# Kernel tuning notes

Hardware: AMD Instinct MI355X
Metric: run time of the kernel (lower is better)

Reference implementation:

```python
import jax, jax.numpy as jnp
import numpy as np

D, H = 1536, 16
HD = D // H            # head_dim = 96
ROPE_CH = HD // 2      # rope_channels_ratio=0.5 -> RoPE on last 48 channels
FF = 4 * D             # SwiGLU hidden
EPS = 1e-6
MAX_WAVELENGTH = 10000.0


def _ln(x):
    # LayerNorm, elementwise_affine=False, eps=1e-6
    m = jnp.mean(x, axis=-1, keepdims=True)
    v = jnp.var(x, axis=-1, keepdims=True)
    return (x - m) * jax.lax.rsqrt(v + EPS)


def _rms(x, w):
    # LlamaRMSNorm: fp32 internally
    xf = x.astype(jnp.float32)
    v = jnp.mean(jnp.square(xf), axis=-1, keepdims=True)
    return (w * (xf * jax.lax.rsqrt(v + EPS))).astype(x.dtype)


def _apply_rope(q, pos):
    # q: [B,H,S,hd], pos: [B,S]
    hd = q.shape[-1]
    frac = 2.0 * jnp.arange(hd // 2, dtype=jnp.float32) / hd
    timescale = MAX_WAVELENGTH ** frac                       # [hd/2]
    sin_inp = pos.astype(jnp.float32)[:, None, :, None] / timescale  # [B,1,S,hd/2]
    sin, cos = jnp.sin(sin_inp), jnp.cos(sin_inp)
    a, b = jnp.split(q, 2, axis=-1)
    out = jnp.concatenate([a * cos - b * sin, b * cos + a * sin], axis=-1)
    return out.astype(q.dtype)


def _rotary(x, pos, ch):
    # apply RoPE to the last `ch` channels of head_dim
    left, right = x[..., :-ch], x[..., -ch:]
    return jnp.concatenate([left, _apply_rope(right, pos)], axis=-1)


def _mod(x, shift, scale):
    # t2i_modulate: x * (1 + scale) + shift, cond broadcast over seq
    return x * (1.0 + scale[:, None, :]) + shift[:, None, :]


def setup_inputs() -> dict:
    key = jax.random.key(0)
    ks = jax.random.split(key, 32)
    B, Nx, Ny = 1, 2048, 256
    w = lambda k, shp: (0.02 * jax.random.normal(k, shp, dtype=jnp.float32))
    inp = {
        'x': jax.random.normal(ks[0], (B, Nx, D), dtype=jnp.float32),
        'y': jax.random.normal(ks[1], (B, Ny, D), dtype=jnp.float32),
        't': jax.random.normal(ks[2], (B, D), dtype=jnp.float32),
        'positions': jnp.arange(Nx, dtype=jnp.int32).reshape(B, Nx),
        'w_mod_x': w(ks[3], (D, 6 * D)), 'b_mod_x': jnp.zeros((6 * D,), jnp.float32),
        'w_mod_y': w(ks[4], (D, 6 * D)), 'b_mod_y': jnp.zeros((6 * D,), jnp.float32),
        'w_qkv_x': w(ks[5], (D, 3 * D)), 'b_qkv_x': jnp.zeros((3 * D,), jnp.float32),
        'w_qkv_y': w(ks[6], (D, 3 * D)), 'b_qkv_y': jnp.zeros((3 * D,), jnp.float32),
        'qn_x': jnp.ones((HD,), jnp.float32), 'kn_x': jnp.ones((HD,), jnp.float32),
        'qn_y': jnp.ones((HD,), jnp.float32), 'kn_y': jnp.ones((HD,), jnp.float32),
        'w_proj_x': w(ks[7], (D, D)), 'b_proj_x': jnp.zeros((D,), jnp.float32),
        'w_proj_y': w(ks[8], (D, D)), 'b_proj_y': jnp.zeros((D,), jnp.float32),
        'w1_x': w(ks[9], (D, FF)), 'w2_x': w(ks[10], (D, FF)), 'w3_x': w(ks[11], (FF, D)),
        'w1_y': w(ks[12], (D, FF)), 'w2_y': w(ks[13], (D, FF)), 'w3_y': w(ks[14], (FF, D)),
    }
    return inp


def reference(x, y, t, positions,
              w_mod_x, b_mod_x, w_mod_y, b_mod_y,
              w_qkv_x, b_qkv_x, w_qkv_y, b_qkv_y,
              qn_x, kn_x, qn_y, kn_y,
              w_proj_x, b_proj_x, w_proj_y, b_proj_y,
              w1_x, w2_x, w3_x, w1_y, w2_y, w3_y):
    B, Nx, _ = x.shape
    Ny = y.shape[1]
    st = jax.nn.silu(t)
    sh1x, sc1x, g1x, sh2x, sc2x, g2x = jnp.split(st @ w_mod_x + b_mod_x, 6, axis=-1)
    sh1y, sc1y, g1y, sh2y, sc2y, g2y = jnp.split(st @ w_mod_y + b_mod_y, 6, axis=-1)

    def qkv(z, w, b, qn, kn, pos):
        q, k, v = jnp.split(z @ w + b, 3, axis=-1)
        r = lambda u: u.reshape(B, -1, H, HD).transpose(0, 2, 1, 3)  # [B,H,S,hd]
        q, k, v = r(q), r(k), r(v)
        q, k = _rms(q, qn), _rms(k, kn)
        if pos is not None:
            q, k = _rotary(q, pos, ROPE_CH), _rotary(k, pos, ROPE_CH)
        return q, k, v

    qx, kx, vx = qkv(_mod(_ln(x), sh1x, sc1x), w_qkv_x, b_qkv_x, qn_x, kn_x, positions)
    qy, ky, vy = qkv(_mod(_ln(y), sh1y, sc1y), w_qkv_y, b_qkv_y, qn_y, kn_y, None)

    q = jnp.concatenate([qx, qy], axis=2)
    k = jnp.concatenate([kx, ky], axis=2)
    v = jnp.concatenate([vx, vy], axis=2)
    scores = jnp.einsum('bhqd,bhkd->bhqk', q, k) * (HD ** -0.5)
    attn = jax.nn.softmax(scores, axis=-1)
    o = jnp.einsum('bhqk,bhkd->bhqd', attn, v)
    o = o.transpose(0, 2, 1, 3).reshape(B, Nx + Ny, D)
    ox, oy = o[:, :Nx], o[:, Nx:]

    x = x + g1x[:, None, :] * (ox @ w_proj_x + b_proj_x)
    y = y + g1y[:, None, :] * (oy @ w_proj_y + b_proj_y)

    def ffn(z, w1, w2, w3):
        return (jax.nn.silu(z @ w1) * (z @ w2)) @ w3

    x = x + g2x[:, None, :] * ffn(_mod(_ln(x), sh2x, sc2x), w1_x, w2_x, w3_x)
    y = y + g2y[:, None, :] * ffn(_mod(_ln(y), sh2y, sc2y), w1_y, w2_y, w3_y)
    return jnp.concatenate([x, y], axis=1)
```

## Files before the change

### kernel.cpp

```cpp
#include <hip/hip_runtime.h>
#include <hip/hip_bf16.h>

#define D_  1536
#define H_  16
#define HD_ 96
#define NX_ 2048
#define NY_ 256
#define NT_ 2304
#define FF_ 6144
#define EPS_ 1e-6f

typedef unsigned short u16;
typedef unsigned int   u32;
typedef short short8 __attribute__((ext_vector_type(8)));
typedef float f32x4  __attribute__((ext_vector_type(4)));
typedef unsigned short u16x4 __attribute__((ext_vector_type(4)));

__device__ __forceinline__ u16 f2bf(float f){
    u32 u = __float_as_uint(f);
    return (u16)((u + 0x7fffu + ((u >> 16) & 1u)) >> 16);
}
__device__ __forceinline__ float bf2f(u16 h){ return __uint_as_float(((u32)h) << 16); }

__device__ __forceinline__ void gll16(const void* g, void* l){
    __builtin_amdgcn_global_load_lds(
        (const __attribute__((address_space(1))) unsigned int*)g,
        (__attribute__((address_space(3))) unsigned int*)l, 16, 0, 0);
}

__global__ __launch_bounds__(256) void transpose_k(
    const float* __restrict__ Wx, const float* __restrict__ Wy,
    u16* __restrict__ Ox, u16* __restrict__ Oy, int K, int N)
{
    const float* W = blockIdx.y ? Wy : Wx;
    u16* O = blockIdx.y ? Oy : Ox;
    int tn_cnt = N >> 5;
    int tk = blockIdx.x / tn_cnt, tn = blockIdx.x % tn_cnt;
    __shared__ float tile[32][33];
    int t = threadIdx.x;
    {
        int k = t >> 3, n4 = (t & 7) * 4;
        float4 v = *(const float4*)&W[(size_t)(tk*32 + k) * N + tn*32 + n4];
        tile[k][n4+0] = v.x; tile[k][n4+1] = v.y;
        tile[k][n4+2] = v.z; tile[k][n4+3] = v.w;
    }
    __syncthreads();
    {
        int n = t >> 3, k4 = (t & 7) * 4;
        u16x4 r;
        #pragma unroll
        for (int i = 0; i < 4; i++) r[i] = f2bf(tile[k4+i][n]);
        *(u16x4*)&O[(size_t)(tn*32 + n) * K + tk*32 + k4] = r;
    }
}

__global__ __launch_bounds__(256) void modvec_k(
    const float* __restrict__ t_in,
    const float* __restrict__ w_mod_x, const float* __restrict__ b_mod_x,
    const float* __restrict__ w_mod_y, const float* __restrict__ b_mod_y,
    float* __restrict__ modx, float* __restrict__ mody)
{
    __shared__ float st[D_];
    int tid = threadIdx.x;
    for (int k = tid; k < D_; k += 256){
        float v = t_in[k];
        st[k] = v / (1.f + __expf(-v));
    }
    __syncthreads();
    int j = blockIdx.x * 256 + tid;
    const float* W; const float* bb; float* out; int col;
    if (j < 6*D_){ W = w_mod_x; bb = b_mod_x; out = modx; col = j; }
    else         { W = w_mod_y; bb = b_mod_y; out = mody; col = j - 6*D_; }
    float acc = bb[col];
    for (int k = 0; k < D_; k++)
        acc += st[k] * W[(size_t)k * (6*D_) + col];
    out[col] = acc;
}

__global__ __launch_bounds__(256) void lnmod_k(
    const float* __restrict__ inx, const float* __restrict__ iny,
    const float* __restrict__ modx, const float* __restrict__ mody,
    int shoff, u16* __restrict__ out)
{
    int row = blockIdx.x, t = threadIdx.x;
    const float* in; const float* mod;
    if (row < NX_){ in = inx + (size_t)row * D_;        mod = modx; }
    else          { in = iny + (size_t)(row-NX_) * D_;  mod = mody; }
    const float* sh = mod + shoff;
    const float* sc = mod + shoff + D_;
    float vals[6]; float s = 0.f, ss = 0.f;
    #pragma unroll
    for (int j = 0; j < 6; j++){
        float v = in[t + j*256];
        vals[j] = v; s += v; ss += v*v;
    }
    for (int mask = 1; mask < 64; mask <<= 1){
        s  += __shfl_xor(s,  mask);
        ss += __shfl_xor(ss, mask);
    }
    __shared__ float red[2][4];
    int wave = t >> 6, lane = t & 63;
    if (lane == 0){ red[0][wave] = s; red[1][wave] = ss; }
    __syncthreads();
    s  = red[0][0] + red[0][1] + red[0][2] + red[0][3];
    ss = red[1][0] + red[1][1] + red[1][2] + red[1][3];
    float mean = s * (1.f / D_);
    float var  = ss * (1.f / D_) - mean * mean;
    float inv  = rsqrtf(var + EPS_);
    #pragma unroll
    for (int j = 0; j < 6; j++){
        int c = t + j*256;
        float z = (vals[j] - mean) * inv;
        z = z * (1.f + sc[c]) + sh[c];
        out[(size_t)row * D_ + c] = f2bf(z);
    }
}

template<int MODE>
__global__ __launch_bounds__(512, 2) void gemm3_k(
    const u16* __restrict__ A,
    const u16* __restrict__ BTx, const u16* __restrict__ BTy,
    const float* __restrict__ biasx, const float* __restrict__ biasy,
    const u16* __restrict__ hmul,
    u16* __restrict__ outB, int ldo,
    int K, int mb, int nb)
{
    __shared__ u16 As[2][256*64];
    __shared__ u16 Bs[2][256*64];
    int nwg = mb * nb;
    int bid = blockIdx.x;
    int q = nwg >> 3, r = nwg & 7, xcd = bid & 7;
    int wgid = (xcd < r ? xcd*(q+1) : r*(q+1) + (xcd - r)*q) + (bid >> 3);
    int bm = wgid % mb, bn = wgid / mb;
    int sel = (bm == mb - 1);
    int row0 = bm * 256, col0 = bn * 256;
    const u16* Bt = sel ? BTy : BTx;

    int t = threadIdx.x, wid = t >> 6, lane = t & 63;
    int lrow = lane & 15, lgrp = lane >> 4;
    int wr = (wid >> 2) * 128, wc = (wid & 3) * 64;

    const char* Ab = (const char*)(A  + (size_t)row0 * K);
    const char* Bb = (const char*)(Bt + (size_t)col0 * K);
    u32 offG[4], offL[4];
    #pragma unroll
    for (int i = 0; i < 4; i++){
        int rr = i*64 + (t >> 3);
        int cc = (t & 7) ^ (rr & 7);
        offG[i] = (u32)(rr * K + cc * 8) * 2;
        offL[i] = (u32)(i*8192 + t*16);
    }

    #define STAGEG(bsel, kb) do{                                                  \
        _Pragma("unroll")                                                         \
        for (int i = 0; i < 4; i++)                                               \
            gll16(Ab + (offG[i] + (kb)), (char*)As[bsel] + offL[i]);              \
        _Pragma("unroll")                                                         \
        for (int i = 0; i < 4; i++)                                               \
            gll16(Bb + (offG[i] + (kb)), (char*)Bs[bsel] + offL[i]);              \
    } while(0)

    f32x4 acc[8][4];
    #pragma unroll
    for (int i = 0; i < 8; i++)
        #pragma unroll
        for (int j = 0; j < 4; j++) acc[i][j] = (f32x4){0.f,0.f,0.f,0.f};

    int nt = K >> 6;
    STAGEG(0, 0);

    for (int tt = 0; tt < nt; tt++){
        const u16* Ac = As[tt & 1];
        const u16* Bc = Bs[tt & 1];
        if (tt + 1 < nt){
            STAGEG((tt + 1) & 1, (u32)(tt + 1) * 128);
            asm volatile("s_waitcnt vmcnt(8)" ::: "memory");
        } else {
            asm volatile("s_waitcnt vmcnt(0)" ::: "memory");
        }
        __builtin_amdgcn_sched_barrier(0);
        __builtin_amdgcn_s_barrier();
        __builtin_amdgcn_sched_barrier(0);
        #pragma unroll
        for (int kk = 0; kk < 2; kk++){
            int pc = ((kk*4 + lgrp) ^ (lrow & 7)) * 8;
            short8 bf[4];
            #pragma unroll
            for (int ni = 0; ni < 4; ni++)
                bf[ni] = *(const short8*)&Bc[(wc + ni*16 + lrow)*64 + pc];
            #pragma unroll
            for (int mi = 0; mi < 8; mi++){
                short8 af = *(const short8*)&Ac[(wr + mi*16 + lrow)*64 + pc];
                #pragma unroll
                for (int ni = 0; ni < 4; ni++)
                    acc[mi][ni] = __builtin_amdgcn_mfma_f32_16x16x32_bf16(
                                      af, bf[ni], acc[mi][ni], 0, 0, 0);
            }
        }
        asm volatile("s_waitcnt lgkmcnt(0)" ::: "memory");
        __builtin_amdgcn_sched_barrier(0);
        __builtin_amdgcn_s_barrier();
        __builtin_amdgcn_sched_barrier(0);
    }
    #undef STAGEG

    const float* biasp = sel ? biasy : biasx;
    #pragma unroll
    for (int mi = 0; mi < 8; mi++){
        #pragma unroll
        for (int ni = 0; ni < 4; ni++){
            #pragma unroll
            for (int rr = 0; rr < 4; rr++){
                int gr = row0 + wr + mi*16 + lgrp*4 + rr;
                int gc = col0 + wc + ni*16 + lrow;
                float v = acc[mi][ni][rr];
                size_t oi = (size_t)gr * ldo + gc;
                if (MODE == 0)      outB[oi] = f2bf(v + biasp[gc]);
                else if (MODE == 2) outB[oi] = f2bf(v / (1.f + __expf(-v)));
                else if (MODE == 3) outB[oi] = f2bf(bf2f(hmul[oi]) * v);
            }
        }
    }
}

template<int MODE>
__global__ __launch_bounds__(256, 2) void gemm2_k(
    const u16* __restrict__ A,
    const u16* __restrict__ BTx, const u16* __restrict__ BTy,
    const float* __restrict__ biasx, const float* __restrict__ biasy,
    const float* __restrict__ residx, const float* __restrict__ residy,
    const float* __restrict__ gmodx, const float* __restrict__ gmody,
    const u16* __restrict__ hmul,
    float* __restrict__ outF, u16* __restrict__ outB, int ldo,
    int K, int nb)
{
    __shared__ u16 As[2][128*64];
    __shared__ u16 Bs[2][128*64];
    int nwg = 18 * nb;
    int bid = blockIdx.x;
    int bid2 = (bid & 7) * (nwg >> 3) + (bid >> 3);
    int bm = bid2 % 18, bn = bid2 / 18;
    int sel = (bm >= 16);
    int row0 = bm * 128, col0 = bn * 128;
    const u16* Bt = sel ? BTy : BTx;

    int t = threadIdx.x, w = t >> 6, l = t & 63;
    int lrow = l & 15, lgrp = l >> 4;
    int wr = (w >> 1) * 64, wc = (w & 1) * 64;

    const char* Ab = (const char*)(A  + (size_t)row0 * K);
    const char* Bb = (const char*)(Bt + (size_t)col0 * K);
    u32 offA[4], ldsoff[4];
    #pragma unroll
    for (int i = 0; i < 4; i++){
        int r = (i*4 + w)*8 + (l >> 3);
        int c = (l & 7) ^ (r & 7);
        offA[i]   = (u32)(r * K + c * 8) * 2;
        ldsoff[i] = (u32)((i*4 + w) * 1024);
    }

    #define STAGEG(bsel, kb) do{                                                  \
        _Pragma("unroll")                                                         \
        for (int i = 0; i < 4; i++)                                               \
            gll16(Ab + (offA[i] + (kb)), (char*)As + (bsel)*16384 + ldsoff[i]);   \
        _Pragma("unroll")                                                         \
        for (int i = 0; i < 4; i++)                                               \
            gll16(Bb + (offA[i] + (kb)), (char*)Bs + (bsel)*16384 + ldsoff[i]);   \
    } while(0)

    f32x4 acc[4][4];
    #pragma unroll
    for (int i = 0; i < 4; i++)
        #pragma unroll
        for (int j = 0; j < 4; j++) acc[i][j] = (f32x4){0.f,0.f,0.f,0.f};

    int nt = K >> 6;
    STAGEG(0, 0);

    for (int tt = 0; tt < nt; tt++){
        const u16* Ac = As[tt & 1];
        const u16* Bc = Bs[tt & 1];
        if (tt + 1 < nt){
            STAGEG((tt + 1) & 1, (u32)(tt + 1) * 128);
            asm volatile("s_waitcnt vmcnt(8)" ::: "memory");
        } else {
            asm volatile("s_waitcnt vmcnt(0)" ::: "memory");
        }
        __builtin_amdgcn_sched_barrier(0);
        __builtin_amdgcn_s_barrier();
        __builtin_amdgcn_sched_barrier(0);
        #pragma unroll
        for (int kk = 0; kk < 2; kk++){
            int pc = ((kk*4 + lgrp) ^ (lrow & 7)) * 8;
            short8 af[4], bf[4];
            #pragma unroll
            for (int mi = 0; mi < 4; mi++)
                af[mi] = *(const short8*)&Ac[(wr + mi*16 + lrow)*64 + pc];
            #pragma unroll
            for (int ni = 0; ni < 4; ni++)
                bf[ni] = *(const short8*)&Bc[(wc + ni*16 + lrow)*64 + pc];
            #pragma unroll
            for (int mi = 0; mi < 4; mi++)
                #pragma unroll
                for (int ni = 0; ni < 4; ni++)
                    acc[mi][ni] = __builtin_amdgcn_mfma_f32_16x16x32_bf16(
                                      af[mi], bf[ni], acc[mi][ni], 0, 0, 0);
        }
        asm volatile("s_waitcnt lgkmcnt(0)" ::: "memory");
        __builtin_amdgcn_sched_barrier(0);
        __builtin_amdgcn_s_barrier();
        __builtin_amdgcn_sched_barrier(0);
    }
    #undef STAGEG

    const float* biasp  = sel ? biasy  : biasx;
    const float* residp = sel ? residy : residx;
    const float* gmodp  = sel ? gmody  : gmodx;
    #pragma unroll
    for (int mi = 0; mi < 4; mi++){
        #pragma unroll
        for (int ni = 0; ni < 4; ni++){
            #pragma unroll
            for (int r = 0; r < 4; r++){
                int gr = row0 + wr + mi*16 + lgrp*4 + r;
                int gc = col0 + wc + ni*16 + lrow;
                float v = acc[mi][ni][r];
                size_t oi = (size_t)gr * ldo + gc;
                if (MODE == 0)      outB[oi] = f2bf(v + biasp[gc]);
                else if (MODE == 1) outF[oi] = residp[oi] + gmodp[gc] * (v + biasp[gc]);
                else if (MODE == 2) outB[oi] = f2bf(v / (1.f + __expf(-v)));
                else if (MODE == 3) outB[oi] = f2bf(bf2f(hmul[oi]) * v);
                else if (MODE == 4) outF[oi] = residp[oi] + gmodp[gc] * v;
            }
        }
    }
}

__global__ __launch_bounds__(256) void qkvpost_k(
    const u16* __restrict__ qkvraw, const int* __restrict__ positions,
    const float* __restrict__ qn_x, const float* __restrict__ kn_x,
    const float* __restrict__ qn_y, const float* __restrict__ kn_y,
    u16* __restrict__ Qg, u16* __restrict__ Kg, u16* __restrict__ Vg)
{
    int tok = blockIdx.x;
    int t = threadIdx.x, wave = t >> 6, lane = t & 63;
    bool isx = tok < NX_;
    float pos = isx ? (float)positions[tok] : 0.f;
    const float* qn = isx ? qn_x : qn_y;
    const float* kn = isx ? kn_x : kn_y;
    bool act = lane < 48;
    int d = lane * 2;
    #pragma unroll
    for (int hh = 0; hh < 4; hh++){
        int h = wave + hh * 4;
        const u16* base = qkvraw + (size_t)tok * (3*D_) + h * HD_;
        float qx=0.f,qy=0.f,kx=0.f,ky=0.f,vx=0.f,vy=0.f;
        if (act){
            u32 qw = *(const u32*)(base + d);
            u32 kw = *(const u32*)(base + D_ + d);
            u32 vw = *(const u32*)(base + 2*D_ + d);
            qx = bf2f((u16)qw); qy = bf2f((u16)(qw >> 16));
            kx = bf2f((u16)kw); ky = bf2f((u16)(kw >> 16));
            vx = bf2f((u16)vw); vy = bf2f((u16)(vw >> 16));
        }
        float sq = qx*qx + qy*qy, sk = kx*kx + ky*ky;
        for (int mask = 1; mask < 64; mask <<= 1){
            sq += __shfl_xor(sq, mask);
            sk += __shfl_xor(sk, mask);
        }
        float rq = rsqrtf(sq / (float)HD_ + EPS_);
        float rk = rsqrtf(sk / (float)HD_ + EPS_);
        if (act){
            qx *= rq * qn[d]; qy *= rq * qn[d+1];
            kx *= rk * kn[d]; ky *= rk * kn[d+1];
        }
        int pl = (lane < 36) ? lane + 12 : lane - 12;
        float qpx = __shfl(qx, pl), qpy = __shfl(qy, pl);
        float kpx = __shfl(kx, pl), kpy = __shfl(ky, pl);
        if (isx && lane >= 24 && act){
            bool aside = lane < 36;
            int i0 = aside ? (2*lane - 48) : (2*lane - 72);
            float ang0 = pos * __powf(10000.f, -(float)i0 / 24.f);
            float ang1 = pos * __powf(10000.f, -(float)(i0+1) / 24.f);
            float s0,c0,s1,c1;
            __sincosf(ang0, &s0, &c0);
            __sincosf(ang1, &s1, &c1);
            if (aside){
                qx = qx*c0 - qpx*s0;  qy = qy*c1 - qpy*s1;
                kx = kx*c0 - kpx*s0;  ky = ky*c1 - kpy*s1;
            } else {
                qx = qx*c0 + qpx*s0;  qy = qy*c1 + qpy*s1;
                kx = kx*c0 + kpx*s0;  ky = ky*c1 + kpy*s1;
            }
        }
        size_t o96  = ((size_t)h * NT_ + tok) * 96;
        size_t o128 = ((size_t)h * NT_ + tok) * 128;
        if (act){
            Qg[o96 + d] = f2bf(qx);  Qg[o96 + d + 1] = f2bf(qy);
            Kg[o128 + d] = f2bf(kx); Kg[o128 + d + 1] = f2bf(ky);
            Vg[o96 + d] = f2bf(vx);  Vg[o96 + d + 1] = f2bf(vy);
        } else {
            int dp = 96 + (lane - 48) * 2;
            Kg[o128 + dp] = 0; Kg[o128 + dp + 1] = 0;
        }
    }
}

__global__ __launch_bounds__(256) void vtrans_k(
    const u16* __restrict__ Vg, u16* __restrict__ Vtg)
{
    int h = blockIdx.y, t0 = blockIdx.x * 64;
    __shared__ u16 tile[64][104];
    int t = threadIdx.x;
    #pragma unroll
    for (int i = 0; i < 3; i++){
        int idx = i*256 + t;
        int tok = idx / 12, c = idx % 12;
        uint4 v = *(const uint4*)&Vg[((size_t)h*NT_ + t0 + tok)*96 + c*8];
        *(uint4*)&tile[tok][c*8] = v;
    }
    __syncthreads();
    #pragma unroll
    for (int i = 0; i < 3; i++){
        int idx = i*256 + t;
        int d = idx >> 3, tc = idx & 7;
        u16 vv[8];
        #pragma unroll
        for (int j = 0; j < 8; j++) vv[j] = tile[tc*8 + j][d];
        *(uint4*)&Vtg[((size_t)h*128 + d)*NT_ + t0 + tc*8] = *(uint4*)vv;
    }
    {
        int row = 96 + (t >> 3), tc = t & 7;
        u16 val = (row == 96) ? (u16)0x3F80 : (u16)0;
        u16 vv[8];
        #pragma unroll
        for (int j = 0; j < 8; j++) vv[j] = val;
        *(uint4*)&Vtg[((size_t)h*128 + row)*NT_ + t0 + tc*8] = *(uint4*)vv;
    }
}

__global__ __launch_bounds__(256, 4) void attn_k(
    const u16* __restrict__ Qg, const u16* __restrict__ Kg,
    const u16* __restrict__ Vtg, u16* __restrict__ Og)
{
    int bid = blockIdx.x;
    int bid2 = (bid & 7) * 72 + (bid >> 3);
    int h = bid2 / 36;
    int q0 = (bid2 % 36) * 64;
    __shared__ u16 Ks[64*128];
    __shared__ u16 Vs[112*64];
    __shared__ u16 Ps[4][16*72];
    int t = threadIdx.x, wave = t >> 6, lane = t & 63;
    int lrow = lane & 15, lgrp = lane >> 4;
    const float C1 = (float)(0.10206207261596577 * 1.4426950408889634);
    const float C2 = (float)(-10.0 * 1.4426950408889634);

    const u16* qbase = Qg + ((size_t)h * NT_ + q0 + wave*16 + lrow) * 96;
    short8 qf[3];
    #pragma unroll
    for (int c = 0; c < 3; c++) qf[c] = *(const short8*)(qbase + c*32 + lgrp*8);

    const u16* Kbh = Kg  + (size_t)h * NT_ * 128;
    const u16* Vbh = Vtg + (size_t)h * 128 * NT_;

    int krow[4], kc_[4], vrow[4], vc_[4];
    #pragma unroll
    for (int i = 0; i < 4; i++){
        int g = wave*4 + i;
        krow[i] = g*4 + (lane >> 4);
        kc_[i]  = (lane & 15) ^ (krow[i] & 7);
        vrow[i] = g*8 + (lane >> 3);
        vc_[i]  = (lane & 7) ^ (vrow[i] & 7);
    }

    f32x4 oacc[7];
    #pragma unroll
    for (int n = 0; n < 7; n++) oacc[n] = (f32x4){0.f,0.f,0.f,0.f};

    for (int kt = 0; kt < NT_/64; kt++){
        __syncthreads();
        #pragma unroll
        for (int i = 0; i < 4; i++)
            gll16(Kbh + ((size_t)(kt*64 + krow[i]))*128 + kc_[i]*8,
                  &Ks[(wave*4 + i)*512 + lane*8]);
        #pragma unroll
        for (int i = 0; i < 4; i++){
            int g = wave*4 + i;
            if (g < 14)
                gll16(Vbh + (size_t)vrow[i]*NT_ + kt*64 + vc_[i]*8,
                      &Vs[g*512 + lane*8]);
        }
        __syncthreads();

        f32x4 s[4];
        #pragma unroll
        for (int nt = 0; nt < 4; nt++){
            s[nt] = (f32x4){0.f,0.f,0.f,0.f};
            #pragma unroll
            for (int c = 0; c < 3; c++){
                int pc = ((c*4 + lgrp) ^ (lrow & 7)) * 8;
                short8 kf = *(const short8*)&Ks[(nt*16 + lrow)*128 + pc];
                s[nt] = __builtin_amdgcn_mfma_f32_16x16x32_bf16(kf, qf[c], s[nt], 0,0,0);
            }
        }
        #pragma unroll
        for (int nt = 0; nt < 4; nt++){
            u32 lo = (u32)f2bf(exp2f(fmaf(s[nt][0], C1, C2)))
                   | ((u32)f2bf(exp2f(fmaf(s[nt][1], C1, C2))) << 16);
            u32 hi = (u32)f2bf(exp2f(fmaf(s[nt][2], C1, C2)))
                   | ((u32)f2bf(exp2f(fmaf(s[nt][3], C1, C2))) << 16);
            uint2 pk; pk.x = lo; pk.y = hi;
            *(uint2*)&Ps[wave][lrow*72 + nt*16 + lgrp*4] = pk;
        }
        #pragma unroll
        for (int kc = 0; kc < 2; kc++){
            short8 pf = *(const short8*)&Ps[wave][lrow*72 + kc*32 + lgrp*8];
            #pragma unroll
            for (int n = 0; n < 7; n++){
                int pc = ((kc*4 + lgrp) ^ (lrow & 7)) * 8;
                short8 vf = *(const short8*)&Vs[(n*16 + lrow)*64 + pc];
                oacc[n] = __builtin_amdgcn_mfma_f32_16x16x32_bf16(pf, vf, oacc[n], 0,0,0);
            }
        }
    }

    float linv[4];
    #pragma unroll
    for (int r = 0; r < 4; r++)
        linv[r] = 1.f / __shfl(oacc[6][r], lane & 48);

    #pragma unroll
    for (int n = 0; n < 6; n++){
        #pragma unroll
        for (int r = 0; r < 4; r++){
            int tok = q0 + wave*16 + lgrp*4 + r;
            Og[(size_t)tok * D_ + h*HD_ + n*16 + lrow] = f2bf(oacc[n][r] * linv[r]);
        }
    }
}

extern "C" void kernel_launch(void* const* d_in, const int* in_sizes, int n_in,
                              void* d_out, int out_size, void* d_ws, size_t ws_size,
                              hipStream_t stream)
{
    const float* x        = (const float*)d_in[0];
    const float* y        = (const float*)d_in[1];
    const float* tt       = (const float*)d_in[2];
    const int*   pos      = (const int*)  d_in[3];
    const float* w_mod_x  = (const float*)d_in[4];
    const float* b_mod_x  = (const float*)d_in[5];
    const float* w_mod_y  = (const float*)d_in[6];
    const float* b_mod_y  = (const float*)d_in[7];
    const float* w_qkv_x  = (const float*)d_in[8];
    const float* b_qkv_x  = (const float*)d_in[9];
    const float* w_qkv_y  = (const float*)d_in[10];
    const float* b_qkv_y  = (const float*)d_in[11];
    const float* qn_x     = (const float*)d_in[12];
    const float* kn_x     = (const float*)d_in[13];
    const float* qn_y     = (const float*)d_in[14];
    const float* kn_y     = (const float*)d_in[15];
    const float* w_proj_x = (const float*)d_in[16];
    const float* b_proj_x = (const float*)d_in[17];
    const float* w_proj_y = (const float*)d_in[18];
    const float* b_proj_y = (const float*)d_in[19];
    const float* w1_x     = (const float*)d_in[20];
    const float* w2_x     = (const float*)d_in[21];
    const float* w3_x     = (const float*)d_in[22];
    const float* w1_y     = (const float*)d_in[23];
    const float* w2_y     = (const float*)d_in[24];
    const float* w3_y     = (const float*)d_in[25];
    float* dout = (float*)d_out;

    char* ws = (char*)d_ws;
    size_t off = 0;
    float* modx   = (float*)(ws + off); off += (size_t)(6*D_) * 4;
    float* mody   = (float*)(ws + off); off += (size_t)(6*D_) * 4;
    u16*   a      = (u16*)  (ws + off); off += (size_t)NT_ * D_ * 2;
    u16*   arena  = (u16*)  (ws + off); off += (size_t)2 * D_ * FF_ * 2;
    u16*   r1     = (u16*)  (ws + off); off += (size_t)NT_ * FF_ * 2;
    u16*   r2     = (u16*)  (ws + off); off += ((size_t)3*96 + 128) * H_ * NT_ * 2;
    float* x1     = (float*)(ws + off); off += (size_t)NT_ * D_ * 4;
    u16*   Vtg    = (u16*)  (ws + off); off += (size_t)H_ * 128 * NT_ * 2;

    u16* qkvraw = r1;
    u16* hs     = r1;
    u16* Qb     = r2;
    u16* Kb     = r2 + (size_t)H_ * NT_ * 96;
    u16* Vb     = r2 + (size_t)H_ * NT_ * (96 + 128);
    u16* Ob     = r2 + (size_t)H_ * NT_ * (2*96 + 128);
    u16* hb     = r2;

    const size_t qkvW  = (size_t)D_ * (3*D_);
    const size_t projW = (size_t)D_ * D_;
    const size_t ffW   = (size_t)D_ * FF_;

    modvec_k<<<72, 256, 0, stream>>>(tt, w_mod_x, b_mod_x, w_mod_y, b_mod_y, modx, mody);
    lnmod_k<<<NT_, 256, 0, stream>>>(x, y, modx, mody, 0, a);
    transpose_k<<<dim3(48*144, 2), 256, 0, stream>>>(w_qkv_x, w_qkv_y, arena, arena + qkvW, D_, 3*D_);
    gemm3_k<0><<<9*18, 512, 0, stream>>>(a, arena, arena + qkvW, b_qkv_x, b_qkv_y,
        nullptr, qkvraw, 3*D_, D_, 9, 18);
    qkvpost_k<<<NT_, 256, 0, stream>>>(qkvraw, pos, qn_x, kn_x, qn_y, kn_y, Qb, Kb, Vb);
    vtrans_k<<<dim3(36, 16), 256, 0, stream>>>(Vb, Vtg);
    attn_k<<<576, 256, 0, stream>>>(Qb, Kb, Vtg, Ob);
    transpose_k<<<dim3(48*48, 2), 256, 0, stream>>>(w_proj_x, w_proj_y, arena, arena + projW, D_, D_);
    gemm2_k<1><<<18*12, 256, 0, stream>>>(Ob, arena, arena + projW, b_proj_x, b_proj_y,
        x, y - (size_t)NX_*D_, modx + 2*D_, mody + 2*D_, nullptr, x1, nullptr, D_, D_, 12);
    lnmod_k<<<NT_, 256, 0, stream>>>(x1, x1 + (size_t)NX_*D_, modx, mody, 3*D_, a);
    transpose_k<<<dim3(48*192, 2), 256, 0, stream>>>(w1_x, w1_y, arena, arena + ffW, D_, FF_);
    gemm3_k<2><<<9*24, 512, 0, stream>>>(a, arena, arena + ffW, nullptr, nullptr,
        nullptr, hs, FF_, D_, 9, 24);
    transpose_k<<<dim3(48*192, 2), 256, 0, stream>>>(w2_x, w2_y, arena, arena + ffW, D_, FF_);
    gemm3_k<3><<<9*24, 512, 0, stream>>>(a, arena, arena + ffW, nullptr, nullptr,
        hs, hb, FF_, D_, 9, 24);
    transpose_k<<<dim3(192*48, 2), 256, 0, stream>>>(w3_x, w3_y, arena, arena + ffW, FF_, D_);
    gemm2_k<4><<<18*12, 256, 0, stream>>>(hb, arena, arena + ffW, nullptr, nullptr,
        x1, x1, modx + 5*D_, mody + 5*D_, nullptr, dout, nullptr, D_, FF_, 12);
    (void)in_sizes; (void)n_in; (void)out_size; (void)ws_size;
}
```

Measured before the change: 584.7 us.

## Fuse SwiGLU up-projections into one GEMM and split-K the down projection

The two FFN up-projection GEMMs (w1 with SiLU, w2 with the gating multiply) are merged into one kernel. It loads each A tile once, accumulates both products and writes only the gated bf16 result, so the intermediate SiLU buffer is no longer written and re-read. The w3 down-projection now runs as a 2-way split-K GEMM that writes fp32 partials, followed by a separate reduce kernel that applies the residual and gate. The cost is a fused kernel holding two accumulator sets at occupancy 1, extra fp32 partial traffic, and a new workspace region for the transposed w2 weights.

```diff
diff --git a/kernel.cpp b/kernel.cpp
--- a/kernel.cpp
+++ b/kernel.cpp
@@ -215,47 +215,51 @@
                 int gc = col0 + wc + ni*16 + lrow;
                 float v = acc[mi][ni][rr];
                 size_t oi = (size_t)gr * ldo + gc;
-                if (MODE == 0)      outB[oi] = f2bf(v + biasp[gc]);
-                else if (MODE == 2) outB[oi] = f2bf(v / (1.f + __expf(-v)));
-                else if (MODE == 3) outB[oi] = f2bf(bf2f(hmul[oi]) * v);
+                if (MODE == 0) outB[oi] = f2bf(v + biasp[gc]);
             }
         }
     }
+    (void)hmul;
 }
 
 template<int MODE>
 __global__ __launch_bounds__(256, 2) void gemm2_k(
-    const u16* __restrict__ A,
-    const u16* __restrict__ BTx, const u16* __restrict__ BTy,
+    const u16* __restrict__ A, int lda,
+    const u16* __restrict__ BTx, const u16* __restrict__ BTy, int ldb,
     const float* __restrict__ biasx, const float* __restrict__ biasy,
     const float* __restrict__ residx, const float* __restrict__ residy,
     const float* __restrict__ gmodx, const float* __restrict__ gmody,
-    const u16* __restrict__ hmul,
-    float* __restrict__ outF, u16* __restrict__ outB, int ldo,
-    int K, int nb)
+    float* __restrict__ outF, int ldo,
+    int K, int nb, int kparts)
 {
     __shared__ u16 As[2][128*64];
     __shared__ u16 Bs[2][128*64];
-    int nwg = 18 * nb;
+    int nwg_base = 18 * nb;
+    int nwg = nwg_base * kparts;
     int bid = blockIdx.x;
     int bid2 = (bid & 7) * (nwg >> 3) + (bid >> 3);
-    int bm = bid2 % 18, bn = bid2 / 18;
+    int ks  = bid2 / nwg_base;
+    int rem = bid2 % nwg_base;
+    int bm = rem % 18, bn = rem / 18;
     int sel = (bm >= 16);
     int row0 = bm * 128, col0 = bn * 128;
-    const u16* Bt = sel ? BTy : BTx;
+    const u16* Bt = (sel ? BTy : BTx) + (size_t)ks * K;
+    const u16* Ap = A + (size_t)ks * K;
+    outF += (size_t)ks * NT_ * D_;
 
     int t = threadIdx.x, w = t >> 6, l = t & 63;
     int lrow = l & 15, lgrp = l >> 4;
     int wr = (w >> 1) * 64, wc = (w & 1) * 64;
 
-    const char* Ab = (const char*)(A  + (size_t)row0 * K);
-    const char* Bb = (const char*)(Bt + (size_t)col0 * K);
-    u32 offA[4], ldsoff[4];
+    const char* Ab = (const char*)(Ap + (size_t)row0 * lda);
+    const char* Bb = (const char*)(Bt + (size_t)col0 * ldb);
+    u32 offA[4], offB[4], ldsoff[4];
     #pragma unroll
     for (int i = 0; i < 4; i++){
         int r = (i*4 + w)*8 + (l >> 3);
         int c = (l & 7) ^ (r & 7);
-        offA[i]   = (u32)(r * K + c * 8) * 2;
+        offA[i]   = (u32)(r * lda + c * 8) * 2;
+        offB[i]   = (u32)(r * ldb + c * 8) * 2;
         ldsoff[i] = (u32)((i*4 + w) * 1024);
     }
 
@@ -265,7 +269,7 @@
             gll16(Ab + (offA[i] + (kb)), (char*)As + (bsel)*16384 + ldsoff[i]);   \
         _Pragma("unroll")                                                         \
         for (int i = 0; i < 4; i++)                                               \
-            gll16(Bb + (offA[i] + (kb)), (char*)Bs + (bsel)*16384 + ldsoff[i]);   \
+            gll16(Bb + (offB[i] + (kb)), (char*)Bs + (bsel)*16384 + ldsoff[i]);   \
     } while(0)
 
     f32x4 acc[4][4];
@@ -326,14 +330,149 @@
                 int gc = col0 + wc + ni*16 + lrow;
                 float v = acc[mi][ni][r];
                 size_t oi = (size_t)gr * ldo + gc;
-                if (MODE == 0)      outB[oi] = f2bf(v + biasp[gc]);
-                else if (MODE == 1) outF[oi] = residp[oi] + gmodp[gc] * (v + biasp[gc]);
-                else if (MODE == 2) outB[oi] = f2bf(v / (1.f + __expf(-v)));
-                else if (MODE == 3) outB[oi] = f2bf(bf2f(hmul[oi]) * v);
-                else if (MODE == 4) outF[oi] = residp[oi] + gmodp[gc] * v;
+                if (MODE == 1)      outF[oi] = residp[oi] + gmodp[gc] * (v + biasp[gc]);
+                else if (MODE == 5) outF[oi] = v;
             }
         }
     }
+}
+
+__global__ __launch_bounds__(256, 1) void ffn12_k(
+    const u16* __restrict__ A,
+    const u16* __restrict__ B1x, const u16* __restrict__ B1y,
+    const u16* __restrict__ B2x, const u16* __restrict__ B2y,
+    u16* __restrict__ outB)
+{
+    __shared__ u16 As[2][128*64];
+    __shared__ u16 B1s[2][128*64];
+    __shared__ u16 B2s[2][128*64];
+    const int K = D_;
+    int nwg = 18 * 48;
+    int bid = blockIdx.x;
+    int bid2 = (bid & 7) * (nwg >> 3) + (bid >> 3);
+    int bm = bid2 % 18, bn = bid2 / 18;
+    int sel = (bm >= 16);
+    int row0 = bm * 128, col0 = bn * 128;
+    const u16* B1 = sel ? B1y : B1x;
+    const u16* B2 = sel ? B2y : B2x;
+
+    int t = threadIdx.x, w = t >> 6, l = t & 63;
+    int lrow = l & 15, lgrp = l >> 4;
+    int wr = (w >> 1) * 64, wc = (w & 1) * 64;
+
+    const char* Ab  = (const char*)(A  + (size_t)row0 * K);
+    const char* B1b = (const char*)(B1 + (size_t)col0 * K);
+    const char* B2b = (const char*)(B2 + (size_t)col0 * K);
+    u32 offA[4], ldsoff[4];
+    #pragma unroll
+    for (int i = 0; i < 4; i++){
+        int r = (i*4 + w)*8 + (l >> 3);
+        int c = (l & 7) ^ (r & 7);
+        offA[i]   = (u32)(r * K + c * 8) * 2;
+        ldsoff[i] = (u32)((i*4 + w) * 1024);
+    }
+
+    #define STAGEF(bsel, kb) do{                                                  \
+        _Pragma("unroll")                                                         \
+        for (int i = 0; i < 4; i++)                                               \
+            gll16(Ab  + (offA[i] + (kb)), (char*)As  + (bsel)*16384 + ldsoff[i]); \
+        _Pragma("unroll")                                                         \
+        for (int i = 0; i < 4; i++)                                               \
+            gll16(B1b + (offA[i] + (kb)), (char*)B1s + (bsel)*16384 + ldsoff[i]); \
+        _Pragma("unroll")                                                         \
+        for (int i = 0; i < 4; i++)                                               \
+            gll16(B2b + (offA[i] + (kb)), (char*)B2s + (bsel)*16384 + ldsoff[i]); \
+    } while(0)
+
+    f32x4 acc1[4][4], acc2[4][4];
+    #pragma unroll
+    for (int i = 0; i < 4; i++)
+        #pragma unroll
+        for (int j = 0; j < 4; j++){
+            acc1[i][j] = (f32x4){0.f,0.f,0.f,0.f};
+            acc2[i][j] = (f32x4){0.f,0.f,0.f,0.f};
+        }
+
+    int nt = K >> 6;
+    STAGEF(0, 0);
+
+    for (int tt = 0; tt < nt; tt++){
+        const u16* Ac  = As[tt & 1];
+        const u16* B1c = B1s[tt & 1];
+        const u16* B2c = B2s[tt & 1];
+        if (tt + 1 < nt){
+            STAGEF((tt + 1) & 1, (u32)(tt + 1) * 128);
+            asm volatile("s_waitcnt vmcnt(12)" ::: "memory");
+        } else {
+            asm volatile("s_waitcnt vmcnt(0)" ::: "memory");
+        }
+        __builtin_amdgcn_sched_barrier(0);
+        __builtin_amdgcn_s_barrier();
+        __builtin_amdgcn_sched_barrier(0);
+        #pragma unroll
+        for (int kk = 0; kk < 2; kk++){
+            int pc = ((kk*4 + lgrp) ^ (lrow & 7)) * 8;
+            short8 af[4], b1f[4], b2f[4];
+            #pragma unroll
+            for (int mi = 0; mi < 4; mi++)
+                af[mi] = *(const short8*)&Ac[(wr + mi*16 + lrow)*64 + pc];
+            #pragma unroll
+            for (int ni = 0; ni < 4; ni++){
+                b1f[ni] = *(const short8*)&B1c[(wc + ni*16 + lrow)*64 + pc];
+                b2f[ni] = *(const short8*)&B2c[(wc + ni*16 + lrow)*64 + pc];
+            }
+            #pragma unroll
+            for (int mi = 0; mi < 4; mi++)
+                #pragma unroll
+                for (int ni = 0; ni < 4; ni++){
+                    acc1[mi][ni] = __builtin_amdgcn_mfma_f32_16x16x32_bf16(
+                                      af[mi], b1f[ni], acc1[mi][ni], 0, 0, 0);
+                    acc2[mi][ni] = __builtin_amdgcn_mfma_f32_16x16x32_bf16(
+                                      af[mi], b2f[ni], acc2[mi][ni], 0, 0, 0);
+                }
+        }
+        asm volatile("s_waitcnt lgkmcnt(0)" ::: "memory");
+        __builtin_amdgcn_sched_barrier(0);
+        __builtin_amdgcn_s_barrier();
+        __builtin_amdgcn_sched_barrier(0);
+    }
+    #undef STAGEF
+
+    #pragma unroll
+    for (int mi = 0; mi < 4; mi++){
+        #pragma unroll
+        for (int ni = 0; ni < 4; ni++){
+            #pragma unroll
+            for (int r = 0; r < 4; r++){
+                int gr = row0 + wr + mi*16 + lgrp*4 + r;
+                int gc = col0 + wc + ni*16 + lrow;
+                float v1 = acc1[mi][ni][r];
+                float v2 = acc2[mi][ni][r];
+                float sv = v1 / (1.f + __expf(-v1));
+                outB[(size_t)gr * FF_ + gc] = f2bf(sv * v2);
+            }
+        }
+    }
+}
+
+__global__ __launch_bounds__(256) void reduce_k(
+    const float* __restrict__ p, const float* __restrict__ x1,
+    const float* __restrict__ modx, const float* __restrict__ mody,
+    float* __restrict__ dout)
+{
+    size_t i = ((size_t)blockIdx.x * 256 + threadIdx.x) * 4;
+    float4 a = *(const float4*)&p[i];
+    float4 b = *(const float4*)&p[(size_t)NT_ * D_ + i];
+    float4 r = *(const float4*)&x1[i];
+    int row = (int)(i / D_), col = (int)(i % D_);
+    const float* g = (row < NX_ ? modx : mody) + 5*D_;
+    float4 gv = *(const float4*)&g[col];
+    float4 o;
+    o.x = r.x + gv.x * (a.x + b.x);
+    o.y = r.y + gv.y * (a.y + b.y);
+    o.z = r.z + gv.z * (a.z + b.z);
+    o.w = r.w + gv.w * (a.w + b.w);
+    *(float4*)&dout[i] = o;
 }
 
 __global__ __launch_bounds__(256) void qkvpost_k(
@@ -580,15 +719,18 @@
     u16*   r1     = (u16*)  (ws + off); off += (size_t)NT_ * FF_ * 2;
     u16*   r2     = (u16*)  (ws + off); off += ((size_t)3*96 + 128) * H_ * NT_ * 2;
     float* x1     = (float*)(ws + off); off += (size_t)NT_ * D_ * 4;
-    u16*   Vtg    = (u16*)  (ws + off); off += (size_t)H_ * 128 * NT_ * 2;
-
-    u16* qkvraw = r1;
-    u16* hs     = r1;
-    u16* Qb     = r2;
-    u16* Kb     = r2 + (size_t)H_ * NT_ * 96;
-    u16* Vb     = r2 + (size_t)H_ * NT_ * (96 + 128);
-    u16* Ob     = r2 + (size_t)H_ * NT_ * (2*96 + 128);
-    u16* hb     = r2;
+    u16*   dreg   = (u16*)  (ws + off); off += (size_t)D_ * FF_ * 2;
+
+    u16*   qkvraw = r1;
+    u16*   w2Tx   = r1;
+    float* p0     = (float*)r1;
+    u16*   Qb     = r2;
+    u16*   Kb     = r2 + (size_t)H_ * NT_ * 96;
+    u16*   Vb     = r2 + (size_t)H_ * NT_ * (96 + 128);
+    u16*   Ob     = r2 + (size_t)H_ * NT_ * (2*96 + 128);
+    u16*   hb     = r2;
+    u16*   Vtg    = dreg;
+    u16*   w2Ty   = dreg;
 
     const size_t qkvW  = (size_t)D_ * (3*D_);
     const size_t projW = (size_t)D_ * D_;
@@ -603,17 +745,17 @@
     vtrans_k<<<dim3(36, 16), 256, 0, stream>>>(Vb, Vtg);
     attn_k<<<576, 256, 0, stream>>>(Qb, Kb, Vtg, Ob);
     transpose_k<<<dim3(48*48, 2), 256, 0, stream>>>(w_proj_x, w_proj_y, arena, arena + projW, D_, D_);
-    gemm2_k<1><<<18*12, 256, 0, stream>>>(Ob, arena, arena + projW, b_proj_x, b_proj_y,
-        x, y - (size_t)NX_*D_, modx + 2*D_, mody + 2*D_, nullptr, x1, nullptr, D_, D_, 12);
+    gemm2_k<1><<<18*12, 256, 0, stream>>>(Ob, D_, arena, arena + projW, D_,
+        b_proj_x, b_proj_y, x, y - (size_t)NX_*D_, modx + 2*D_, mody + 2*D_,
+        x1, D_, D_, 12, 1);
     lnmod_k<<<NT_, 256, 0, stream>>>(x1, x1 + (size_t)NX_*D_, modx, mody, 3*D_, a);
     transpose_k<<<dim3(48*192, 2), 256, 0, stream>>>(w1_x, w1_y, arena, arena + ffW, D_, FF_);
-    gemm3_k<2><<<9*24, 512, 0, stream>>>(a, arena, arena + ffW, nullptr, nullptr,
-        nullptr, hs, FF_, D_, 9, 24);
-    transpose_k<<<dim3(48*192, 2), 256, 0, stream>>>(w2_x, w2_y, arena, arena + ffW, D_, FF_);
-    gemm3_k<3><<<9*24, 512, 0, stream>>>(a, arena, arena + ffW, nullptr, nullptr,
-        hs, hb, FF_, D_, 9, 24);
+    transpose_k<<<dim3(48*192, 2), 256, 0, stream>>>(w2_x, w2_y, w2Tx, w2Ty, D_, FF_);
+    ffn12_k<<<18*48, 256, 0, stream>>>(a, arena, arena + ffW, w2Tx, w2Ty, hb);
     transpose_k<<<dim3(192*48, 2), 256, 0, stream>>>(w3_x, w3_y, arena, arena + ffW, FF_, D_);
-    gemm2_k<4><<<18*12, 256, 0, stream>>>(hb, arena, arena + ffW, nullptr, nullptr,
-        x1, x1, modx + 5*D_, mody + 5*D_, nullptr, dout, nullptr, D_, FF_, 12);
+    gemm2_k<5><<<18*12*2, 256, 0, stream>>>(hb, FF_, arena, arena + ffW, FF_,
+        nullptr, nullptr, nullptr, nullptr, nullptr, nullptr,
+        p0, D_, 3072, 12, 2);
+    reduce_k<<<(NT_*D_/4)/256, 256, 0, stream>>>(p0, x1, modx, mody, dout);
     (void)in_sizes; (void)n_in; (void)out_size; (void)ws_size;
 }
```

Result: slower. 602.5 us (+3.1%).

## Split-K the FFN down-projection GEMM into two partials plus a reduce kernel

Applied to the files above, without the earlier changes.

The final FFN GEMM (K=6144) now launches twice as many workgroups, each covering half of K and writing fp32 partial sums to the workspace. A new elementwise kernel adds the two partials and applies the gated residual. The aim is better CU occupancy, since the original 216-workgroup grid underfills the GPU. The cost is an extra fp32 write and read of two NT×D buffers and one more launch.

```diff
diff --git a/kernel.cpp b/kernel.cpp
--- a/kernel.cpp
+++ b/kernel.cpp
@@ -225,37 +225,42 @@
 
 template<int MODE>
 __global__ __launch_bounds__(256, 2) void gemm2_k(
-    const u16* __restrict__ A,
-    const u16* __restrict__ BTx, const u16* __restrict__ BTy,
+    const u16* __restrict__ A, int lda,
+    const u16* __restrict__ BTx, const u16* __restrict__ BTy, int ldb,
     const float* __restrict__ biasx, const float* __restrict__ biasy,
     const float* __restrict__ residx, const float* __restrict__ residy,
     const float* __restrict__ gmodx, const float* __restrict__ gmody,
-    const u16* __restrict__ hmul,
-    float* __restrict__ outF, u16* __restrict__ outB, int ldo,
-    int K, int nb)
+    float* __restrict__ outF, int ldo,
+    int K, int nb, int kparts)
 {
     __shared__ u16 As[2][128*64];
     __shared__ u16 Bs[2][128*64];
-    int nwg = 18 * nb;
+    int nwg_base = 18 * nb;
+    int nwg = nwg_base * kparts;
     int bid = blockIdx.x;
     int bid2 = (bid & 7) * (nwg >> 3) + (bid >> 3);
-    int bm = bid2 % 18, bn = bid2 / 18;
+    int ks  = bid2 / nwg_base;
+    int rem = bid2 % nwg_base;
+    int bm = rem % 18, bn = rem / 18;
     int sel = (bm >= 16);
     int row0 = bm * 128, col0 = bn * 128;
-    const u16* Bt = sel ? BTy : BTx;
+    const u16* Bt = (sel ? BTy : BTx) + (size_t)ks * K;
+    const u16* Ap = A + (size_t)ks * K;
+    outF += (size_t)ks * NT_ * D_;
 
     int t = threadIdx.x, w = t >> 6, l = t & 63;
     int lrow = l & 15, lgrp = l >> 4;
     int wr = (w >> 1) * 64, wc = (w & 1) * 64;
 
-    const char* Ab = (const char*)(A  + (size_t)row0 * K);
-    const char* Bb = (const char*)(Bt + (size_t)col0 * K);
-    u32 offA[4], ldsoff[4];
+    const char* Ab = (const char*)(Ap + (size_t)row0 * lda);
+    const char* Bb = (const char*)(Bt + (size_t)col0 * ldb);
+    u32 offA[4], offB[4], ldsoff[4];
     #pragma unroll
     for (int i = 0; i < 4; i++){
         int r = (i*4 + w)*8 + (l >> 3);
         int c = (l & 7) ^ (r & 7);
-        offA[i]   = (u32)(r * K + c * 8) * 2;
+        offA[i]   = (u32)(r * lda + c * 8) * 2;
+        offB[i]   = (u32)(r * ldb + c * 8) * 2;
         ldsoff[i] = (u32)((i*4 + w) * 1024);
     }
 
@@ -265,7 +270,7 @@
             gll16(Ab + (offA[i] + (kb)), (char*)As + (bsel)*16384 + ldsoff[i]);   \
         _Pragma("unroll")                                                         \
         for (int i = 0; i < 4; i++)                                               \
-            gll16(Bb + (offA[i] + (kb)), (char*)Bs + (bsel)*16384 + ldsoff[i]);   \
+            gll16(Bb + (offB[i] + (kb)), (char*)Bs + (bsel)*16384 + ldsoff[i]);   \
     } while(0)
 
     f32x4 acc[4][4];
@@ -326,14 +331,31 @@
                 int gc = col0 + wc + ni*16 + lrow;
                 float v = acc[mi][ni][r];
                 size_t oi = (size_t)gr * ldo + gc;
-                if (MODE == 0)      outB[oi] = f2bf(v + biasp[gc]);
-                else if (MODE == 1) outF[oi] = residp[oi] + gmodp[gc] * (v + biasp[gc]);
-                else if (MODE == 2) outB[oi] = f2bf(v / (1.f + __expf(-v)));
-                else if (MODE == 3) outB[oi] = f2bf(bf2f(hmul[oi]) * v);
-                else if (MODE == 4) outF[oi] = residp[oi] + gmodp[gc] * v;
+                if (MODE == 1)      outF[oi] = residp[oi] + gmodp[gc] * (v + biasp[gc]);
+                else if (MODE == 5) outF[oi] = v;
             }
         }
     }
+}
+
+__global__ __launch_bounds__(256) void reduce_k(
+    const float* __restrict__ p, const float* __restrict__ x1,
+    const float* __restrict__ modx, const float* __restrict__ mody,
+    float* __restrict__ dout)
+{
+    size_t i = ((size_t)blockIdx.x * 256 + threadIdx.x) * 4;
+    float4 a = *(const float4*)&p[i];
+    float4 b = *(const float4*)&p[(size_t)NT_ * D_ + i];
+    float4 r = *(const float4*)&x1[i];
+    int row = (int)(i / D_), col = (int)(i % D_);
+    const float* g = (row < NX_ ? modx : mody) + 5*D_;
+    float4 gv = *(const float4*)&g[col];
+    float4 o;
+    o.x = r.x + gv.x * (a.x + b.x);
+    o.y = r.y + gv.y * (a.y + b.y);
+    o.z = r.z + gv.z * (a.z + b.z);
+    o.w = r.w + gv.w * (a.w + b.w);
+    *(float4*)&dout[i] = o;
 }
 
 __global__ __launch_bounds__(256) void qkvpost_k(
@@ -582,13 +604,14 @@
     float* x1     = (float*)(ws + off); off += (size_t)NT_ * D_ * 4;
     u16*   Vtg    = (u16*)  (ws + off); off += (size_t)H_ * 128 * NT_ * 2;
 
-    u16* qkvraw = r1;
-    u16* hs     = r1;
-    u16* Qb     = r2;
-    u16* Kb     = r2 + (size_t)H_ * NT_ * 96;
-    u16* Vb     = r2 + (size_t)H_ * NT_ * (96 + 128);
-    u16* Ob     = r2 + (size_t)H_ * NT_ * (2*96 + 128);
-    u16* hb     = r2;
+    u16*   qkvraw = r1;
+    u16*   hs     = r1;
+    float* p0     = (float*)r1;
+    u16*   Qb     = r2;
+    u16*   Kb     = r2 + (size_t)H_ * NT_ * 96;
+    u16*   Vb     = r2 + (size_t)H_ * NT_ * (96 + 128);
+    u16*   Ob     = r2 + (size_t)H_ * NT_ * (2*96 + 128);
+    u16*   hb     = r2;
 
     const size_t qkvW  = (size_t)D_ * (3*D_);
     const size_t projW = (size_t)D_ * D_;
@@ -603,8 +626,9 @@
     vtrans_k<<<dim3(36, 16), 256, 0, stream>>>(Vb, Vtg);
     attn_k<<<576, 256, 0, stream>>>(Qb, Kb, Vtg, Ob);
     transpose_k<<<dim3(48*48, 2), 256, 0, stream>>>(w_proj_x, w_proj_y, arena, arena + projW, D_, D_);
-    gemm2_k<1><<<18*12, 256, 0, stream>>>(Ob, arena, arena + projW, b_proj_x, b_proj_y,
-        x, y - (size_t)NX_*D_, modx + 2*D_, mody + 2*D_, nullptr, x1, nullptr, D_, D_, 12);
+    gemm2_k<1><<<18*12, 256, 0, stream>>>(Ob, D_, arena, arena + projW, D_,
+        b_proj_x, b_proj_y, x, y - (size_t)NX_*D_, modx + 2*D_, mody + 2*D_,
+        x1, D_, D_, 12, 1);
     lnmod_k<<<NT_, 256, 0, stream>>>(x1, x1 + (size_t)NX_*D_, modx, mody, 3*D_, a);
     transpose_k<<<dim3(48*192, 2), 256, 0, stream>>>(w1_x, w1_y, arena, arena + ffW, D_, FF_);
     gemm3_k<2><<<9*24, 512, 0, stream>>>(a, arena, arena + ffW, nullptr, nullptr,
@@ -613,7 +637,9 @@
     gemm3_k<3><<<9*24, 512, 0, stream>>>(a, arena, arena + ffW, nullptr, nullptr,
         hs, hb, FF_, D_, 9, 24);
     transpose_k<<<dim3(192*48, 2), 256, 0, stream>>>(w3_x, w3_y, arena, arena + ffW, FF_, D_);
-    gemm2_k<4><<<18*12, 256, 0, stream>>>(hb, arena, arena + ffW, nullptr, nullptr,
-        x1, x1, modx + 5*D_, mody + 5*D_, nullptr, dout, nullptr, D_, FF_, 12);
+    gemm2_k<5><<<18*12*2, 256, 0, stream>>>(hb, FF_, arena, arena + ffW, FF_,
+        nullptr, nullptr, nullptr, nullptr, nullptr, nullptr,
+        p0, D_, 3072, 12, 2);
+    reduce_k<<<(NT_*D_/4)/256, 256, 0, stream>>>(p0, x1, modx, mody, dout);
     (void)in_sizes; (void)n_in; (void)out_size; (void)ws_size;
 }
```

New measurement: 541.7 us. -7.4%, faster.
